# Performance work log

Measured on AMD Instinct MI355X. Metric: run time of the kernel, lower is better.

Reference implementation:

```python
import jax, jax.numpy as jnp
import numpy as np

B, T, H, NUM_LAYERS = 256, 1024, 128, 2


def _lstm_layer(x, W_ih, W_hh, b_ih, b_hh):
    """Single LSTM layer, PyTorch gate order (i, f, g, o).
    x: [B, T, in], W_ih: [4H, in], W_hh: [4H, H], biases: [4H]. Returns [B, T, H].
    """
    Bv = x.shape[0]
    Hv = W_hh.shape[1]
    # Precompute input-to-gate projections for all timesteps (big GEMM outside scan)
    xg = jnp.einsum('bti,gi->btg', x, W_ih) + b_ih + b_hh  # [B, T, 4H]

    def step(carry, xg_t):
        h, c = carry
        g = xg_t + h @ W_hh.T  # [B, 4H]
        i, f, gg, o = jnp.split(g, 4, axis=-1)
        i = jax.nn.sigmoid(i)
        f = jax.nn.sigmoid(f)
        gg = jnp.tanh(gg)
        o = jax.nn.sigmoid(o)
        c = f * c + i * gg
        h = o * jnp.tanh(c)
        return (h, c), h

    h0 = jnp.zeros((Bv, Hv), x.dtype)
    c0 = jnp.zeros((Bv, Hv), x.dtype)
    _, hs = jax.lax.scan(step, (h0, c0), jnp.swapaxes(xg, 0, 1))  # hs: [T, B, H]
    return jnp.swapaxes(hs, 0, 1)


def setup_inputs() -> dict:
    key = jax.random.key(0)
    ks = jax.random.split(key, 11)
    s = 1.0 / np.sqrt(H)  # PyTorch LSTM init scale
    inp = {
        'x': jax.random.normal(ks[0], (B, T, 1), dtype=jnp.float32),
        'W_ih0': jax.random.uniform(ks[1], (4 * H, 1), minval=-s, maxval=s, dtype=jnp.float32),
        'W_hh0': jax.random.uniform(ks[2], (4 * H, H), minval=-s, maxval=s, dtype=jnp.float32),
        'b_ih0': jax.random.uniform(ks[3], (4 * H,), minval=-s, maxval=s, dtype=jnp.float32),
        'b_hh0': jax.random.uniform(ks[4], (4 * H,), minval=-s, maxval=s, dtype=jnp.float32),
        'W_ih1': jax.random.uniform(ks[5], (4 * H, H), minval=-s, maxval=s, dtype=jnp.float32),
        'W_hh1': jax.random.uniform(ks[6], (4 * H, H), minval=-s, maxval=s, dtype=jnp.float32),
        'b_ih1': jax.random.uniform(ks[7], (4 * H,), minval=-s, maxval=s, dtype=jnp.float32),
        'b_hh1': jax.random.uniform(ks[8], (4 * H,), minval=-s, maxval=s, dtype=jnp.float32),
        'fc_w': jax.random.uniform(ks[9], (1, H), minval=-s, maxval=s, dtype=jnp.float32),
        'fc_b': jax.random.uniform(ks[10], (1,), minval=-s, maxval=s, dtype=jnp.float32),
    }
    return inp


def reference(x, W_ih0, W_hh0, b_ih0, b_hh0, W_ih1, W_hh1, b_ih1, b_hh1, fc_w, fc_b):
    h = _lstm_layer(x, W_ih0, W_hh0, b_ih0, b_hh0)   # [B, T, H]
    h = _lstm_layer(h, W_ih1, W_hh1, b_ih1, b_hh1)   # [B, T, H]
    out = jnp.einsum('bth,oh->bto', h, fc_w) + fc_b  # [B, T, 1]
    return out
```

## Files before the change

kernel.cpp:

```cpp
#include <hip/hip_runtime.h>

#define TT 1024
#define HH 128

typedef unsigned int u32;
typedef unsigned short u16;
typedef _Float16 f16;
typedef f16 f16x2 __attribute__((ext_vector_type(2)));
typedef f16 f16x8 __attribute__((ext_vector_type(8)));
typedef float f32x4 __attribute__((ext_vector_type(4)));
typedef u32 u32x4 __attribute__((ext_vector_type(4)));

#define MFMA16(A, B, C) __builtin_amdgcn_mfma_f32_16x16x32_f16((A), (B), (C), 0, 0, 0)
#define K2L2E 2.8853900817779268f

__device__ __forceinline__ float ex2(float x) {
#if __has_builtin(__builtin_amdgcn_exp2f)
    return __builtin_amdgcn_exp2f(x);
#else
    extern "C" __device__ float __ocml_exp2_f32(float);
    return __ocml_exp2_f32(x);
#endif
}
__device__ __forceinline__ float rcp_(float x) { return __builtin_amdgcn_rcpf(x); }

__device__ __forceinline__ float fdot2_(u32 w, u32 h, float acc) {
#if __has_builtin(__builtin_amdgcn_fdot2)
    return __builtin_amdgcn_fdot2(__builtin_bit_cast(f16x2, w),
                                  __builtin_bit_cast(f16x2, h), acc, false);
#else
    const f16x2 a = __builtin_bit_cast(f16x2, w);
    const f16x2 b = __builtin_bit_cast(f16x2, h);
    return fmaf((float)a.y, (float)b.y, fmaf((float)a.x, (float)b.x, acc));
#endif
}

__device__ __forceinline__ float dpp_mov(float v, const int ctrl) {
    int t;
    switch (ctrl) {
      case 0x00: t = __builtin_amdgcn_update_dpp(0, __float_as_int(v), 0x00, 0xF, 0xF, true); break;
      case 0x55: t = __builtin_amdgcn_update_dpp(0, __float_as_int(v), 0x55, 0xF, 0xF, true); break;
      case 0xAA: t = __builtin_amdgcn_update_dpp(0, __float_as_int(v), 0xAA, 0xF, 0xF, true); break;
      default:   t = __builtin_amdgcn_update_dpp(0, __float_as_int(v), 0xFF, 0xF, 0xF, true); break;
    }
    return __int_as_float(t);
}
__device__ __forceinline__ float dpp_add(float v, const int ctrl) {
    int t;
    switch (ctrl) {
      case 0xB1:  t = __builtin_amdgcn_update_dpp(0, __float_as_int(v), 0xB1,  0xF, 0xF, true); break;
      case 0x4E:  t = __builtin_amdgcn_update_dpp(0, __float_as_int(v), 0x4E,  0xF, 0xF, true); break;
      default:    t = __builtin_amdgcn_update_dpp(0, __float_as_int(v), 0x141, 0xF, 0xF, true); break;
    }
    return v + __int_as_float(t);
}
__device__ __forceinline__ float red8(float v) {
    v = dpp_add(v, 0xB1); v = dpp_add(v, 0x4E); v = dpp_add(v, 0x141);
    return v;
}

__global__ void prep(const float* __restrict__ Whh0, const float* __restrict__ Whh1,
                     const float* __restrict__ Wih1, const float* __restrict__ Wih0,
                     const float* __restrict__ bih0, const float* __restrict__ bhh0,
                     const float* __restrict__ bih1, const float* __restrict__ bhh1,
                     f16* __restrict__ Wpk0, f16* __restrict__ Wpk1,
                     f16* __restrict__ W1h,  f16* __restrict__ W1l,
                     float* __restrict__ bx0, float* __restrict__ wx0,
                     float* __restrict__ b1p)
{
    const int p = blockIdx.x;
    const int k = threadIdx.x;
    const int c = p & 3, u = p >> 2;
    const int g = c * 128 + u;
    const float sc = (c == 2) ? K2L2E : -1.4426950408889634f;

    Wpk0[p * HH + k] = (f16)(Whh0[(size_t)g * HH + k] * sc);
    Wpk1[p * HH + k] = (f16)(Whh1[(size_t)g * HH + k] * sc);
    const float wf = Wih1[(size_t)g * HH + k] * sc;
    const f16 wh = (f16)wf;
    W1h[p * HH + k] = wh;
    W1l[p * HH + k] = (f16)(wf - (float)wh);
    if (k == 0) {
        bx0[p] = (bih0[g] + bhh0[g]) * sc;
        wx0[p] = Wih0[g] * sc;
        b1p[p] = (bih1[g] + bhh1[g]) * sc;
    }
}

__global__ __launch_bounds__(512, 2) void lstm0(
    const float* __restrict__ x, const f16* __restrict__ Wpk0,
    const float* __restrict__ bx0, const float* __restrict__ wx0,
    f16* __restrict__ h0g)
{
    const int b = blockIdx.x;
    const int tid = threadIdx.x;
    const int u = tid >> 2;
    const bool lead = (tid & 3) == 0;
    const bool is_g = (tid & 3) == 2;
    const float Ag = is_g ? -2.f : 1.f;
    const float Cg = is_g ?  1.f : 0.f;

    __shared__ __align__(16) float xS[TT];
    __shared__ __align__(16) u32 hS[2][64];
    __shared__ __align__(16) u16 hO[32][HH];

    xS[tid] = x[(size_t)b * TT + tid];
    xS[tid + 512] = x[(size_t)b * TT + tid + 512];
    if (tid < 128) hS[0][tid & 63] = 0u;

    u32x4 Wv[16];
    {
        const u32* wp = (const u32*)(Wpk0 + (size_t)tid * HH);
#pragma unroll
        for (int r = 0; r < 16; ++r) Wv[r] = *(const u32x4*)(wp + r * 4);
    }
    const float biasx = bx0[tid];
    const float wxv = wx0[tid];
    float c1 = 0.f;
    __syncthreads();

    f16* og = h0g + (size_t)b * TT * HH;

#pragma unroll 1
    for (int t0 = 0; t0 < TT; t0 += 32) {
#pragma unroll 1
        for (int i = 0; i < 32; ++i) {
            const int t = t0 + i;
            const u32* hcur = hS[t & 1];
            float a0 = 0.f, a1 = 0.f;
#pragma unroll
            for (int r = 0; r < 16; ++r) {
                const u32x4 hq = *(const u32x4*)(hcur + r * 4);
                a0 = fdot2_(Wv[r].x, hq.x, a0);
                a1 = fdot2_(Wv[r].y, hq.y, a1);
                a0 = fdot2_(Wv[r].z, hq.z, a0);
                a1 = fdot2_(Wv[r].w, hq.w, a1);
            }
            const float a = a0 + a1 + fmaf(xS[t], wxv, biasx);
            const float act = fmaf(Ag, rcp_(1.f + ex2(a)), Cg);
            const float gi = dpp_mov(act, 0x00);
            const float gf = dpp_mov(act, 0x55);
            const float gg = dpp_mov(act, 0xAA);
            const float go = dpp_mov(act, 0xFF);
            c1 = fmaf(gf, c1, gi * gg);
            const float h = go * fmaf(-2.f, rcp_(1.f + ex2(K2L2E * c1)), 1.f);
            if (lead) {
                const u16 hb = __builtin_bit_cast(u16, (f16)h);
                ((u16*)hS[(t + 1) & 1])[u] = hb;
                hO[i][u] = hb;
            }
            __syncthreads();
        }
        *(u32x4*)((u16*)og + (size_t)t0 * HH + tid * 8) = *(const u32x4*)(&hO[0][0] + tid * 8);
        __syncthreads();
    }
}

__global__ __launch_bounds__(512, 2) void lstm1(
    const f16* __restrict__ h0g, const f16* __restrict__ Wpk1,
    const f16* __restrict__ W1h, const f16* __restrict__ W1l,
    const float* __restrict__ b1p, const float* __restrict__ fcw,
    const float* __restrict__ fcb, float* __restrict__ out)
{
    const int b = blockIdx.x;
    const int tid = threadIdx.x;
    const int u = tid >> 2;
    const int wv = tid >> 6;
    const int lane = tid & 63;
    const int lr = lane & 15, lq = lane >> 4;
    const bool lead = (tid & 3) == 0;
    const bool is_g = (tid & 3) == 2;
    const float Ag = is_g ? -2.f : 1.f;
    const float Cg = is_g ?  1.f : 0.f;

    __shared__ __align__(16) float xgS[32 * 512];
    __shared__ __align__(16) u32 hS[2][64];
    __shared__ __align__(16) float fcP[2][8];

    if (tid < 128) hS[0][tid & 63] = 0u;
    const float fcwv = fcw[u];
    const float fcbv = fcb[0];
    const int bp_addr = ((lane ^ 32) << 2);
    float c1 = 0.f;
    __syncthreads();

    const f16* hb0 = h0g + (size_t)b * TT * HH;
    float* ob = out + (size_t)b * TT;

#pragma unroll 1
    for (int t0 = 0; t0 < TT; t0 += 32) {
        {
            f16x8 B0[4], B1[4];
#pragma unroll
            for (int ks = 0; ks < 4; ++ks) {
                B0[ks] = *(const f16x8*)(hb0 + (size_t)(t0 + lr) * HH + ks * 32 + lq * 8);
                B1[ks] = *(const f16x8*)(hb0 + (size_t)(t0 + 16 + lr) * HH + ks * 32 + lq * 8);
            }
#pragma unroll
            for (int gtl = 0; gtl < 4; ++gtl) {
                const int g16 = (wv * 4 + gtl) * 16;
                const float4 bi = *(const float4*)&b1p[g16 + lq * 4];
                f32x4 a0 = {bi.x, bi.y, bi.z, bi.w};
                f32x4 a1 = a0;
#pragma unroll
                for (int ks = 0; ks < 4; ++ks) {
                    const f16x8 Ah = *(const f16x8*)(W1h + (size_t)(g16 + lr) * HH + ks * 32 + lq * 8);
                    const f16x8 Al = *(const f16x8*)(W1l + (size_t)(g16 + lr) * HH + ks * 32 + lq * 8);
                    a0 = MFMA16(Ah, B0[ks], a0);
                    a0 = MFMA16(Al, B0[ks], a0);
                    a1 = MFMA16(Ah, B1[ks], a1);
                    a1 = MFMA16(Al, B1[ks], a1);
                }
                const int gb = g16 + lq * 4;
                *(f32x4*)&xgS[lr * 512 + (gb ^ ((lr & 7) << 2))] = a0;
                *(f32x4*)&xgS[(16 + lr) * 512 + (gb ^ (((16 + lr) & 7) << 2))] = a1;
            }
        }
        __syncthreads();

        u32x4 Wv[16];
        {
            const u32* wp = (const u32*)(Wpk1 + (size_t)tid * HH);
            asm volatile("" : "+v"(wp));
#pragma unroll
            for (int r = 0; r < 16; ++r) Wv[r] = *(const u32x4*)(wp + r * 4);
        }

#pragma unroll 1
        for (int i = 0; i < 32; ++i) {
            const int t = t0 + i;
            if (wv == 7 && t > 0) {
                float v = (lane < 8) ? fcP[(t & 1) ^ 1][lane] : 0.f;
                v = red8(v);
                if (lane == 0) ob[t - 1] = v + fcbv;
            }
            const u32* hcur = hS[t & 1];
            float a0 = 0.f, a1 = 0.f;
#pragma unroll
            for (int r = 0; r < 16; ++r) {
                const u32x4 hq = *(const u32x4*)(hcur + r * 4);
                a0 = fdot2_(Wv[r].x, hq.x, a0);
                a1 = fdot2_(Wv[r].y, hq.y, a1);
                a0 = fdot2_(Wv[r].z, hq.z, a0);
                a1 = fdot2_(Wv[r].w, hq.w, a1);
            }
            const float a = a0 + a1 + xgS[i * 512 + (tid ^ ((i & 7) << 2))];
            const float act = fmaf(Ag, rcp_(1.f + ex2(a)), Cg);
            const float gi = dpp_mov(act, 0x00);
            const float gf = dpp_mov(act, 0x55);
            const float gg = dpp_mov(act, 0xAA);
            const float go = dpp_mov(act, 0xFF);
            c1 = fmaf(gf, c1, gi * gg);
            const float h = go * fmaf(-2.f, rcp_(1.f + ex2(K2L2E * c1)), 1.f);
            if (lead) ((u16*)hS[(t + 1) & 1])[u] = __builtin_bit_cast(u16, (f16)h);
            float pf = lead ? h * fcwv : 0.f;
            pf = red8(pf);
            pf += __int_as_float(__builtin_amdgcn_ds_swizzle(__float_as_int(pf), 0x201F));
            pf += __int_as_float(__builtin_amdgcn_ds_swizzle(__float_as_int(pf), 0x401F));
            pf += __int_as_float(__builtin_amdgcn_ds_bpermute(bp_addr, __float_as_int(pf)));
            if (lane == 0) fcP[t & 1][wv] = pf;
            __syncthreads();
        }
    }
    if (wv == 7) {
        float v = (lane < 8) ? fcP[(TT - 1) & 1][lane] : 0.f;
        v = red8(v);
        if (lane == 0) ob[TT - 1] = v + fcbv;
    }
}

extern "C" void kernel_launch(void* const* d_in, const int* in_sizes, int n_in,
                              void* d_out, int out_size, void* d_ws, size_t ws_size,
                              hipStream_t stream)
{
    const float* x    = (const float*)d_in[0];
    const float* Wih0 = (const float*)d_in[1];
    const float* Whh0 = (const float*)d_in[2];
    const float* bih0 = (const float*)d_in[3];
    const float* bhh0 = (const float*)d_in[4];
    const float* Wih1 = (const float*)d_in[5];
    const float* Whh1 = (const float*)d_in[6];
    const float* bih1 = (const float*)d_in[7];
    const float* bhh1 = (const float*)d_in[8];
    const float* fcw  = (const float*)d_in[9];
    const float* fcb  = (const float*)d_in[10];
    float* out = (float*)d_out;

    f16* h0g  = (f16*)d_ws;
    f16* Wpk0 = h0g + (size_t)256 * TT * HH;
    f16* Wpk1 = Wpk0 + 512 * HH;
    f16* W1h  = Wpk1 + 512 * HH;
    f16* W1l  = W1h + 512 * HH;
    float* bx0 = (float*)(W1l + 512 * HH);
    float* wx0 = bx0 + 512;
    float* b1p = wx0 + 512;

    prep <<<512, 128, 0, stream>>>(Whh0, Whh1, Wih1, Wih0, bih0, bhh0, bih1, bhh1,
                                   Wpk0, Wpk1, W1h, W1l, bx0, wx0, b1p);
    lstm0<<<256, 512, 0, stream>>>(x, Wpk0, bx0, wx0, h0g);
    lstm1<<<256, 512, 0, stream>>>(h0g, Wpk1, W1h, W1l, b1p, fcw, fcb, out);
}
```

Before: 1.447 ms.

## Fuse both LSTM layers into one wavefront-pipelined kernel

Merges the two per-layer recurrent kernels into one kernel that runs layer 0 on chunk c while layer 1 runs on chunk c-1. Both layers advance inside the same per-timestep barrier. Layer-0 hidden states stay in shared memory (swizzled) and feed the MFMA input projection directly, removing the global h0 round trip and one long serial kernel. The cost is twice the register weights per thread, occupancy bound dropping to 1 block per CU, and more work per barrier step. The fc output reduction is also moved to read h1 from shared memory one step later.

Result: slower. 1.533 ms (+6.0%).

```diff
diff --git a/kernel.cpp b/kernel.cpp
--- a/kernel.cpp
+++ b/kernel.cpp
@@ -87,114 +87,136 @@
     }
 }
 
-__global__ __launch_bounds__(512, 2) void lstm0(
-    const float* __restrict__ x, const f16* __restrict__ Wpk0,
-    const float* __restrict__ bx0, const float* __restrict__ wx0,
-    f16* __restrict__ h0g)
-{
-    const int b = blockIdx.x;
-    const int tid = threadIdx.x;
-    const int u = tid >> 2;
-    const bool lead = (tid & 3) == 0;
-    const bool is_g = (tid & 3) == 2;
-    const float Ag = is_g ? -2.f : 1.f;
-    const float Cg = is_g ?  1.f : 0.f;
-
-    __shared__ __align__(16) float xS[TT];
-    __shared__ __align__(16) u32 hS[2][64];
-    __shared__ __align__(16) u16 hO[32][HH];
-
-    xS[tid] = x[(size_t)b * TT + tid];
-    xS[tid + 512] = x[(size_t)b * TT + tid + 512];
-    if (tid < 128) hS[0][tid & 63] = 0u;
-
-    u32x4 Wv[16];
-    {
-        const u32* wp = (const u32*)(Wpk0 + (size_t)tid * HH);
-#pragma unroll
-        for (int r = 0; r < 16; ++r) Wv[r] = *(const u32x4*)(wp + r * 4);
-    }
-    const float biasx = bx0[tid];
-    const float wxv = wx0[tid];
-    float c1 = 0.f;
-    __syncthreads();
-
-    f16* og = h0g + (size_t)b * TT * HH;
-
-#pragma unroll 1
-    for (int t0 = 0; t0 < TT; t0 += 32) {
-#pragma unroll 1
-        for (int i = 0; i < 32; ++i) {
-            const int t = t0 + i;
-            const u32* hcur = hS[t & 1];
-            float a0 = 0.f, a1 = 0.f;
-#pragma unroll
-            for (int r = 0; r < 16; ++r) {
-                const u32x4 hq = *(const u32x4*)(hcur + r * 4);
-                a0 = fdot2_(Wv[r].x, hq.x, a0);
-                a1 = fdot2_(Wv[r].y, hq.y, a1);
-                a0 = fdot2_(Wv[r].z, hq.z, a0);
-                a1 = fdot2_(Wv[r].w, hq.w, a1);
-            }
-            const float a = a0 + a1 + fmaf(xS[t], wxv, biasx);
-            const float act = fmaf(Ag, rcp_(1.f + ex2(a)), Cg);
-            const float gi = dpp_mov(act, 0x00);
-            const float gf = dpp_mov(act, 0x55);
-            const float gg = dpp_mov(act, 0xAA);
-            const float go = dpp_mov(act, 0xFF);
-            c1 = fmaf(gf, c1, gi * gg);
-            const float h = go * fmaf(-2.f, rcp_(1.f + ex2(K2L2E * c1)), 1.f);
-            if (lead) {
-                const u16 hb = __builtin_bit_cast(u16, (f16)h);
-                ((u16*)hS[(t + 1) & 1])[u] = hb;
-                hO[i][u] = hb;
-            }
-            __syncthreads();
-        }
-        *(u32x4*)((u16*)og + (size_t)t0 * HH + tid * 8) = *(const u32x4*)(&hO[0][0] + tid * 8);
-        __syncthreads();
-    }
-}
-
-__global__ __launch_bounds__(512, 2) void lstm1(
-    const f16* __restrict__ h0g, const f16* __restrict__ Wpk1,
-    const f16* __restrict__ W1h, const f16* __restrict__ W1l,
+__global__ __launch_bounds__(512, 1) void lstm_fused(
+    const float* __restrict__ x,
+    const f16* __restrict__ Wpk0, const float* __restrict__ bx0,
+    const float* __restrict__ wx0, const f16* __restrict__ Wpk1,
+    const f16* __restrict__ W1h,  const f16* __restrict__ W1l,
     const float* __restrict__ b1p, const float* __restrict__ fcw,
     const float* __restrict__ fcb, float* __restrict__ out)
 {
     const int b = blockIdx.x;
     const int tid = threadIdx.x;
     const int u = tid >> 2;
-    const int wv = tid >> 6;
-    const int lane = tid & 63;
+    const int wv = tid >> 6, lane = tid & 63;
     const int lr = lane & 15, lq = lane >> 4;
     const bool lead = (tid & 3) == 0;
     const bool is_g = (tid & 3) == 2;
     const float Ag = is_g ? -2.f : 1.f;
     const float Cg = is_g ?  1.f : 0.f;
 
+    __shared__ __align__(16) float xS[TT];
     __shared__ __align__(16) float xgS[32 * 512];
-    __shared__ __align__(16) u32 hS[2][64];
-    __shared__ __align__(16) float fcP[2][8];
-
-    if (tid < 128) hS[0][tid & 63] = 0u;
-    const float fcwv = fcw[u];
-    const float fcbv = fcb[0];
+    __shared__ __align__(16) u16 h0c[32][HH];
+    __shared__ __align__(16) u32 hS0[2][64];
+    __shared__ __align__(16) u32 hS1[2][64];
+
+    xS[tid]       = x[(size_t)b * TT + tid];
+    xS[tid + 512] = x[(size_t)b * TT + tid + 512];
+    if (tid < 64) { hS0[0][tid] = 0u; hS0[1][tid] = 0u; hS1[0][tid] = 0u; hS1[1][tid] = 0u; }
+
+    u32x4 W0[16], W1r[16];
+    {
+        const u32* wp0 = (const u32*)(Wpk0 + (size_t)tid * HH);
+        const u32* wp1 = (const u32*)(Wpk1 + (size_t)tid * HH);
+#pragma unroll
+        for (int r = 0; r < 16; ++r) {
+            W0[r]  = *(const u32x4*)(wp0 + r * 4);
+            W1r[r] = *(const u32x4*)(wp1 + r * 4);
+        }
+    }
+    const float biasx = bx0[tid];
+    const float wxv   = wx0[tid];
+    const float2 fc2  = *(const float2*)&fcw[2 * lane];
+    const float fcbv  = fcb[0];
     const int bp_addr = ((lane ^ 32) << 2);
-    float c1 = 0.f;
+    float c0 = 0.f, c1 = 0.f;
+    float* ob = out + (size_t)b * TT;
     __syncthreads();
 
-    const f16* hb0 = h0g + (size_t)b * TT * HH;
-    float* ob = out + (size_t)b * TT;
-
 #pragma unroll 1
-    for (int t0 = 0; t0 < TT; t0 += 32) {
-        {
+    for (int cc = 0; cc < 33; ++cc) {
+        const bool l0act = cc < 32;
+        const bool l1act = cc > 0;
+        const int t0 = cc * 32;
+
+#pragma unroll 1
+        for (int i = 0; i < 32; ++i) {
+            const int cur = i & 1, nxt = cur ^ 1;
+            const int t1 = t0 - 32 + i;
+
+            if (l1act && wv == 7 && t1 > 0) {
+                const f16x2 hp = __builtin_bit_cast(f16x2, hS1[cur][lane]);
+                float pf = fmaf((float)hp.y, fc2.y, (float)hp.x * fc2.x);
+                pf = red8(pf);
+                pf += __int_as_float(__builtin_amdgcn_ds_swizzle(__float_as_int(pf), 0x201F));
+                pf += __int_as_float(__builtin_amdgcn_ds_swizzle(__float_as_int(pf), 0x401F));
+                pf += __int_as_float(__builtin_amdgcn_ds_bpermute(bp_addr, __float_as_int(pf)));
+                if (lane == 0) ob[t1 - 1] = pf + fcbv;
+            }
+
+            float h0v = 0.f;
+            if (l0act) {
+                const u32* hcur = hS0[cur];
+                float a0 = 0.f, a1 = 0.f, a2 = 0.f, a3 = 0.f;
+#pragma unroll
+                for (int r = 0; r < 16; ++r) {
+                    const u32x4 hq = *(const u32x4*)(hcur + r * 4);
+                    a0 = fdot2_(W0[r].x, hq.x, a0);
+                    a1 = fdot2_(W0[r].y, hq.y, a1);
+                    a2 = fdot2_(W0[r].z, hq.z, a2);
+                    a3 = fdot2_(W0[r].w, hq.w, a3);
+                }
+                const float a = (a0 + a1) + (a2 + a3) + fmaf(xS[t0 + i], wxv, biasx);
+                const float act = fmaf(Ag, rcp_(1.f + ex2(a)), Cg);
+                const float gi = dpp_mov(act, 0x00);
+                const float gf = dpp_mov(act, 0x55);
+                const float gg = dpp_mov(act, 0xAA);
+                const float go = dpp_mov(act, 0xFF);
+                c0 = fmaf(gf, c0, gi * gg);
+                h0v = go * fmaf(-2.f, rcp_(1.f + ex2(K2L2E * c0)), 1.f);
+            }
+
+            float h1v = 0.f;
+            if (l1act) {
+                const float xgv = xgS[i * 512 + (tid ^ ((i & 7) << 2))];
+                const u32* hcur = hS1[cur];
+                float a0 = 0.f, a1 = 0.f, a2 = 0.f, a3 = 0.f;
+#pragma unroll
+                for (int r = 0; r < 16; ++r) {
+                    const u32x4 hq = *(const u32x4*)(hcur + r * 4);
+                    a0 = fdot2_(W1r[r].x, hq.x, a0);
+                    a1 = fdot2_(W1r[r].y, hq.y, a1);
+                    a2 = fdot2_(W1r[r].z, hq.z, a2);
+                    a3 = fdot2_(W1r[r].w, hq.w, a3);
+                }
+                const float a = (a0 + a1) + (a2 + a3) + xgv;
+                const float act = fmaf(Ag, rcp_(1.f + ex2(a)), Cg);
+                const float gi = dpp_mov(act, 0x00);
+                const float gf = dpp_mov(act, 0x55);
+                const float gg = dpp_mov(act, 0xAA);
+                const float go = dpp_mov(act, 0xFF);
+                c1 = fmaf(gf, c1, gi * gg);
+                h1v = go * fmaf(-2.f, rcp_(1.f + ex2(K2L2E * c1)), 1.f);
+            }
+
+            if (l0act && lead) {
+                const u16 hb = __builtin_bit_cast(u16, (f16)h0v);
+                ((u16*)hS0[nxt])[u] = hb;
+                h0c[i][u ^ ((i & 7) << 3)] = hb;
+            }
+            if (l1act && lead)
+                ((u16*)hS1[nxt])[u] = __builtin_bit_cast(u16, (f16)h1v);
+            __syncthreads();
+        }
+
+        if (l0act) {
             f16x8 B0[4], B1[4];
 #pragma unroll
             for (int ks = 0; ks < 4; ++ks) {
-                B0[ks] = *(const f16x8*)(hb0 + (size_t)(t0 + lr) * HH + ks * 32 + lq * 8);
-                B1[ks] = *(const f16x8*)(hb0 + (size_t)(t0 + 16 + lr) * HH + ks * 32 + lq * 8);
+                const int kb = (ks * 32 + lq * 8) ^ ((lr & 7) << 3);
+                B0[ks] = *(const f16x8*)&h0c[lr][kb];
+                B1[ks] = *(const f16x8*)&h0c[16 + lr][kb];
             }
 #pragma unroll
             for (int gtl = 0; gtl < 4; ++gtl) {
@@ -213,59 +235,20 @@
                 }
                 const int gb = g16 + lq * 4;
                 *(f32x4*)&xgS[lr * 512 + (gb ^ ((lr & 7) << 2))] = a0;
-                *(f32x4*)&xgS[(16 + lr) * 512 + (gb ^ (((16 + lr) & 7) << 2))] = a1;
+                *(f32x4*)&xgS[(16 + lr) * 512 + (gb ^ ((lr & 7) << 2))] = a1;
             }
         }
         __syncthreads();
-
-        u32x4 Wv[16];
-        {
-            const u32* wp = (const u32*)(Wpk1 + (size_t)tid * HH);
-            asm volatile("" : "+v"(wp));
-#pragma unroll
-            for (int r = 0; r < 16; ++r) Wv[r] = *(const u32x4*)(wp + r * 4);
-        }
-
-#pragma unroll 1
-        for (int i = 0; i < 32; ++i) {
-            const int t = t0 + i;
-            if (wv == 7 && t > 0) {
-                float v = (lane < 8) ? fcP[(t & 1) ^ 1][lane] : 0.f;
-                v = red8(v);
-                if (lane == 0) ob[t - 1] = v + fcbv;
-            }
-            const u32* hcur = hS[t & 1];
-            float a0 = 0.f, a1 = 0.f;
-#pragma unroll
-            for (int r = 0; r < 16; ++r) {
-                const u32x4 hq = *(const u32x4*)(hcur + r * 4);
-                a0 = fdot2_(Wv[r].x, hq.x, a0);
-                a1 = fdot2_(Wv[r].y, hq.y, a1);
-                a0 = fdot2_(Wv[r].z, hq.z, a0);
-                a1 = fdot2_(Wv[r].w, hq.w, a1);
-            }
-            const float a = a0 + a1 + xgS[i * 512 + (tid ^ ((i & 7) << 2))];
-            const float act = fmaf(Ag, rcp_(1.f + ex2(a)), Cg);
-            const float gi = dpp_mov(act, 0x00);
-            const float gf = dpp_mov(act, 0x55);
-            const float gg = dpp_mov(act, 0xAA);
-            const float go = dpp_mov(act, 0xFF);
-            c1 = fmaf(gf, c1, gi * gg);
-            const float h = go * fmaf(-2.f, rcp_(1.f + ex2(K2L2E * c1)), 1.f);
-            if (lead) ((u16*)hS[(t + 1) & 1])[u] = __builtin_bit_cast(u16, (f16)h);
-            float pf = lead ? h * fcwv : 0.f;
-            pf = red8(pf);
-            pf += __int_as_float(__builtin_amdgcn_ds_swizzle(__float_as_int(pf), 0x201F));
-            pf += __int_as_float(__builtin_amdgcn_ds_swizzle(__float_as_int(pf), 0x401F));
-            pf += __int_as_float(__builtin_amdgcn_ds_bpermute(bp_addr, __float_as_int(pf)));
-            if (lane == 0) fcP[t & 1][wv] = pf;
-            __syncthreads();
-        }
-    }
+    }
+
     if (wv == 7) {
-        float v = (lane < 8) ? fcP[(TT - 1) & 1][lane] : 0.f;
-        v = red8(v);
-        if (lane == 0) ob[TT - 1] = v + fcbv;
+        const f16x2 hp = __builtin_bit_cast(f16x2, hS1[0][lane]);
+        float pf = fmaf((float)hp.y, fc2.y, (float)hp.x * fc2.x);
+        pf = red8(pf);
+        pf += __int_as_float(__builtin_amdgcn_ds_swizzle(__float_as_int(pf), 0x201F));
+        pf += __int_as_float(__builtin_amdgcn_ds_swizzle(__float_as_int(pf), 0x401F));
+        pf += __int_as_float(__builtin_amdgcn_ds_bpermute(bp_addr, __float_as_int(pf)));
+        if (lane == 0) ob[TT - 1] = pf + fcbv;
     }
 }
 
@@ -286,8 +269,7 @@
     const float* fcb  = (const float*)d_in[10];
     float* out = (float*)d_out;
 
-    f16* h0g  = (f16*)d_ws;
-    f16* Wpk0 = h0g + (size_t)256 * TT * HH;
+    f16* Wpk0 = (f16*)d_ws;
     f16* Wpk1 = Wpk0 + 512 * HH;
     f16* W1h  = Wpk1 + 512 * HH;
     f16* W1l  = W1h + 512 * HH;
@@ -295,8 +277,8 @@
     float* wx0 = bx0 + 512;
     float* b1p = wx0 + 512;
 
-    prep <<<512, 128, 0, stream>>>(Whh0, Whh1, Wih1, Wih0, bih0, bhh0, bih1, bhh1,
-                                   Wpk0, Wpk1, W1h, W1l, bx0, wx0, b1p);
-    lstm0<<<256, 512, 0, stream>>>(x, Wpk0, bx0, wx0, h0g);
-    lstm1<<<256, 512, 0, stream>>>(h0g, Wpk1, W1h, W1l, b1p, fcw, fcb, out);
-}
+    prep<<<512, 128, 0, stream>>>(Whh0, Whh1, Wih1, Wih0, bih0, bhh0, bih1, bhh1,
+                                  Wpk0, Wpk1, W1h, W1l, bx0, wx0, b1p);
+    lstm_fused<<<256, 512, 0, stream>>>(x, Wpk0, bx0, wx0, Wpk1, W1h, W1l, b1p,
+                                        fcw, fcb, out);
+}
```

## Split recurrent dot products across quad lanes with DPP transpose-reduce, batch FC output

Applied to the files above, without the earlier changes.

Each thread in a 4-lane group now computes partial dot products over one quarter of K for all four gates of its hidden unit, then combines them with a DPP butterfly transpose-reduce. Before, each thread ran a full 128-long K loop for a single gate. The hidden-state LDS layout is swizzled so the four lanes read different banks, and layer 0's step loop is flattened. In layer 1, the per-step FC reduction drops the ds_bpermute and serial wave-7 output and instead writes partials per step, which 32 threads sum once per 32-step chunk. This aims to shorten the serial per-step dependency chain at the cost of extra DPP shuffles and selects.

Measured after the change: 1.269 ms. 12.3% less time.

```diff
diff --git a/kernel.cpp b/kernel.cpp
--- a/kernel.cpp
+++ b/kernel.cpp
@@ -41,7 +41,9 @@
       case 0x00: t = __builtin_amdgcn_update_dpp(0, __float_as_int(v), 0x00, 0xF, 0xF, true); break;
       case 0x55: t = __builtin_amdgcn_update_dpp(0, __float_as_int(v), 0x55, 0xF, 0xF, true); break;
       case 0xAA: t = __builtin_amdgcn_update_dpp(0, __float_as_int(v), 0xAA, 0xF, 0xF, true); break;
-      default:   t = __builtin_amdgcn_update_dpp(0, __float_as_int(v), 0xFF, 0xF, 0xF, true); break;
+      case 0xFF: t = __builtin_amdgcn_update_dpp(0, __float_as_int(v), 0xFF, 0xF, 0xF, true); break;
+      case 0xB1: t = __builtin_amdgcn_update_dpp(0, __float_as_int(v), 0xB1, 0xF, 0xF, true); break;
+      default:   t = __builtin_amdgcn_update_dpp(0, __float_as_int(v), 0x4E, 0xF, 0xF, true); break;
     }
     return __int_as_float(t);
 }
@@ -50,13 +52,30 @@
     switch (ctrl) {
       case 0xB1:  t = __builtin_amdgcn_update_dpp(0, __float_as_int(v), 0xB1,  0xF, 0xF, true); break;
       case 0x4E:  t = __builtin_amdgcn_update_dpp(0, __float_as_int(v), 0x4E,  0xF, 0xF, true); break;
-      default:    t = __builtin_amdgcn_update_dpp(0, __float_as_int(v), 0x141, 0xF, 0xF, true); break;
+      case 0x141: t = __builtin_amdgcn_update_dpp(0, __float_as_int(v), 0x141, 0xF, 0xF, true); break;
+      default:    t = __builtin_amdgcn_update_dpp(0, __float_as_int(v), 0x140, 0xF, 0xF, true); break;
     }
     return v + __int_as_float(t);
 }
-__device__ __forceinline__ float red8(float v) {
-    v = dpp_add(v, 0xB1); v = dpp_add(v, 0x4E); v = dpp_add(v, 0x141);
-    return v;
+
+__device__ __forceinline__ int hswz(int iu) {
+    return (iu & 0x30) + (((((iu >> 2) & 3) + (iu >> 4)) & 3) << 2) + (iu & 3);
+}
+
+__device__ __forceinline__ float xpose4(float a0, float a1, float a2, float a3, int q) {
+    const bool qb0 = (q & 1) != 0;
+    float s0, s1;
+    {
+        const float send = qb0 ? a0 : a1;
+        s0 = (qb0 ? a1 : a0) + dpp_mov(send, 0xB1);
+    }
+    {
+        const float send = qb0 ? a2 : a3;
+        s1 = (qb0 ? a3 : a2) + dpp_mov(send, 0xB1);
+    }
+    const bool qb1 = (q & 2) != 0;
+    const float send = qb1 ? s0 : s1;
+    return (qb1 ? s1 : s0) + dpp_mov(send, 0x4E);
 }
 
 __global__ void prep(const float* __restrict__ Whh0, const float* __restrict__ Whh1,
@@ -94,9 +113,8 @@
 {
     const int b = blockIdx.x;
     const int tid = threadIdx.x;
-    const int u = tid >> 2;
-    const bool lead = (tid & 3) == 0;
-    const bool is_g = (tid & 3) == 2;
+    const int u = tid >> 2, q = tid & 3;
+    const bool is_g = (q == 2);
     const float Ag = is_g ? -2.f : 1.f;
     const float Cg = is_g ?  1.f : 0.f;
 
@@ -104,55 +122,60 @@
     __shared__ __align__(16) u32 hS[2][64];
     __shared__ __align__(16) u16 hO[32][HH];
 
-    xS[tid] = x[(size_t)b * TT + tid];
+    xS[tid]       = x[(size_t)b * TT + tid];
     xS[tid + 512] = x[(size_t)b * TT + tid + 512];
-    if (tid < 128) hS[0][tid & 63] = 0u;
-
-    u32x4 Wv[16];
-    {
-        const u32* wp = (const u32*)(Wpk0 + (size_t)tid * HH);
-#pragma unroll
-        for (int r = 0; r < 16; ++r) Wv[r] = *(const u32x4*)(wp + r * 4);
+    if (tid < 128) ((u32*)hS)[tid] = 0u;
+
+    u32x4 Wq[4][4];
+#pragma unroll
+    for (int c = 0; c < 4; ++c) {
+        const u32* wp = (const u32*)Wpk0 + (size_t)((tid & ~3) + c) * 64 + q * 16;
+#pragma unroll
+        for (int rb = 0; rb < 4; ++rb) Wq[c][rb] = *(const u32x4*)(wp + rb * 4);
     }
     const float biasx = bx0[tid];
-    const float wxv = wx0[tid];
+    const float wxv   = wx0[tid];
     float c1 = 0.f;
     __syncthreads();
 
     f16* og = h0g + (size_t)b * TT * HH;
 
 #pragma unroll 1
-    for (int t0 = 0; t0 < TT; t0 += 32) {
-#pragma unroll 1
-        for (int i = 0; i < 32; ++i) {
-            const int t = t0 + i;
-            const u32* hcur = hS[t & 1];
-            float a0 = 0.f, a1 = 0.f;
-#pragma unroll
-            for (int r = 0; r < 16; ++r) {
-                const u32x4 hq = *(const u32x4*)(hcur + r * 4);
-                a0 = fdot2_(Wv[r].x, hq.x, a0);
-                a1 = fdot2_(Wv[r].y, hq.y, a1);
-                a0 = fdot2_(Wv[r].z, hq.z, a0);
-                a1 = fdot2_(Wv[r].w, hq.w, a1);
-            }
-            const float a = a0 + a1 + fmaf(xS[t], wxv, biasx);
-            const float act = fmaf(Ag, rcp_(1.f + ex2(a)), Cg);
-            const float gi = dpp_mov(act, 0x00);
-            const float gf = dpp_mov(act, 0x55);
-            const float gg = dpp_mov(act, 0xAA);
-            const float go = dpp_mov(act, 0xFF);
-            c1 = fmaf(gf, c1, gi * gg);
-            const float h = go * fmaf(-2.f, rcp_(1.f + ex2(K2L2E * c1)), 1.f);
-            if (lead) {
-                const u16 hb = __builtin_bit_cast(u16, (f16)h);
-                ((u16*)hS[(t + 1) & 1])[u] = hb;
-                hO[i][u] = hb;
-            }
+    for (int t = 0; t < TT; ++t) {
+        const u32* hcur = hS[t & 1];
+        float a0 = 0.f, a1 = 0.f, a2 = 0.f, a3 = 0.f;
+#pragma unroll
+        for (int rb = 0; rb < 4; ++rb) {
+            const u32x4 hq = *(const u32x4*)(hcur + (q << 4) + (((rb + q) & 3) << 2));
+            a0 = fdot2_(Wq[0][rb].x, hq.x, a0); a0 = fdot2_(Wq[0][rb].y, hq.y, a0);
+            a0 = fdot2_(Wq[0][rb].z, hq.z, a0); a0 = fdot2_(Wq[0][rb].w, hq.w, a0);
+            a1 = fdot2_(Wq[1][rb].x, hq.x, a1); a1 = fdot2_(Wq[1][rb].y, hq.y, a1);
+            a1 = fdot2_(Wq[1][rb].z, hq.z, a1); a1 = fdot2_(Wq[1][rb].w, hq.w, a1);
+            a2 = fdot2_(Wq[2][rb].x, hq.x, a2); a2 = fdot2_(Wq[2][rb].y, hq.y, a2);
+            a2 = fdot2_(Wq[2][rb].z, hq.z, a2); a2 = fdot2_(Wq[2][rb].w, hq.w, a2);
+            a3 = fdot2_(Wq[3][rb].x, hq.x, a3); a3 = fdot2_(Wq[3][rb].y, hq.y, a3);
+            a3 = fdot2_(Wq[3][rb].z, hq.z, a3); a3 = fdot2_(Wq[3][rb].w, hq.w, a3);
+        }
+        const float V = xpose4(a0, a1, a2, a3, q);
+        const float a = V + fmaf(xS[t], wxv, biasx);
+        const float act = fmaf(Ag, rcp_(1.f + ex2(a)), Cg);
+        const float gi = dpp_mov(act, 0x00);
+        const float gf = dpp_mov(act, 0x55);
+        const float gg = dpp_mov(act, 0xAA);
+        const float go = dpp_mov(act, 0xFF);
+        c1 = fmaf(gf, c1, gi * gg);
+        const float h = go * fmaf(-2.f, rcp_(1.f + ex2(K2L2E * c1)), 1.f);
+        if (q == 0) {
+            const u16 hb = __builtin_bit_cast(u16, (f16)h);
+            ((u16*)hS[(t + 1) & 1])[2 * hswz(u >> 1) + (u & 1)] = hb;
+            hO[t & 31][u] = hb;
+        }
+        __syncthreads();
+        if ((t & 31) == 31) {
+            *(u32x4*)((u16*)og + (size_t)(t - 31) * HH + tid * 8) =
+                *(const u32x4*)(&hO[0][0] + tid * 8);
             __syncthreads();
         }
-        *(u32x4*)((u16*)og + (size_t)t0 * HH + tid * 8) = *(const u32x4*)(&hO[0][0] + tid * 8);
-        __syncthreads();
     }
 }
 
@@ -164,23 +187,20 @@
 {
     const int b = blockIdx.x;
     const int tid = threadIdx.x;
-    const int u = tid >> 2;
-    const int wv = tid >> 6;
-    const int lane = tid & 63;
+    const int u = tid >> 2, q = tid & 3;
+    const int wv = tid >> 6, lane = tid & 63;
     const int lr = lane & 15, lq = lane >> 4;
-    const bool lead = (tid & 3) == 0;
-    const bool is_g = (tid & 3) == 2;
+    const bool is_g = (q == 2);
     const float Ag = is_g ? -2.f : 1.f;
     const float Cg = is_g ?  1.f : 0.f;
 
     __shared__ __align__(16) float xgS[32 * 512];
-    __shared__ __align__(16) u32 hS[2][64];
-    __shared__ __align__(16) float fcP[2][8];
-
-    if (tid < 128) hS[0][tid & 63] = 0u;
-    const float fcwv = fcw[u];
+    __shared__ __align__(16) u32 hS1[2][64];
+    __shared__ __align__(16) float fcP[32][16];
+
+    if (tid < 128) ((u32*)hS1)[tid] = 0u;
+    const float fcu025 = fcw[u] * 0.25f;
     const float fcbv = fcb[0];
-    const int bp_addr = ((lane ^ 32) << 2);
     float c1 = 0.f;
     __syncthreads();
 
@@ -213,38 +233,42 @@
                 }
                 const int gb = g16 + lq * 4;
                 *(f32x4*)&xgS[lr * 512 + (gb ^ ((lr & 7) << 2))] = a0;
-                *(f32x4*)&xgS[(16 + lr) * 512 + (gb ^ (((16 + lr) & 7) << 2))] = a1;
+                *(f32x4*)&xgS[(16 + lr) * 512 + (gb ^ ((lr & 7) << 2))] = a1;
             }
         }
         __syncthreads();
 
-        u32x4 Wv[16];
+        u32x4 Wq[4][4];
         {
-            const u32* wp = (const u32*)(Wpk1 + (size_t)tid * HH);
-            asm volatile("" : "+v"(wp));
-#pragma unroll
-            for (int r = 0; r < 16; ++r) Wv[r] = *(const u32x4*)(wp + r * 4);
+            const u32* wb = (const u32*)Wpk1;
+            asm volatile("" : "+v"(wb));
+#pragma unroll
+            for (int c = 0; c < 4; ++c) {
+                const u32* wp = wb + (size_t)((tid & ~3) + c) * 64 + q * 16;
+#pragma unroll
+                for (int rb = 0; rb < 4; ++rb) Wq[c][rb] = *(const u32x4*)(wp + rb * 4);
+            }
         }
 
 #pragma unroll 1
         for (int i = 0; i < 32; ++i) {
             const int t = t0 + i;
-            if (wv == 7 && t > 0) {
-                float v = (lane < 8) ? fcP[(t & 1) ^ 1][lane] : 0.f;
-                v = red8(v);
-                if (lane == 0) ob[t - 1] = v + fcbv;
-            }
-            const u32* hcur = hS[t & 1];
-            float a0 = 0.f, a1 = 0.f;
-#pragma unroll
-            for (int r = 0; r < 16; ++r) {
-                const u32x4 hq = *(const u32x4*)(hcur + r * 4);
-                a0 = fdot2_(Wv[r].x, hq.x, a0);
-                a1 = fdot2_(Wv[r].y, hq.y, a1);
-                a0 = fdot2_(Wv[r].z, hq.z, a0);
-                a1 = fdot2_(Wv[r].w, hq.w, a1);
-            }
-            const float a = a0 + a1 + xgS[i * 512 + (tid ^ ((i & 7) << 2))];
+            const u32* hcur = hS1[t & 1];
+            float a0 = 0.f, a1 = 0.f, a2 = 0.f, a3 = 0.f;
+#pragma unroll
+            for (int rb = 0; rb < 4; ++rb) {
+                const u32x4 hq = *(const u32x4*)(hcur + (q << 4) + (((rb + q) & 3) << 2));
+                a0 = fdot2_(Wq[0][rb].x, hq.x, a0); a0 = fdot2_(Wq[0][rb].y, hq.y, a0);
+                a0 = fdot2_(Wq[0][rb].z, hq.z, a0); a0 = fdot2_(Wq[0][rb].w, hq.w, a0);
+                a1 = fdot2_(Wq[1][rb].x, hq.x, a1); a1 = fdot2_(Wq[1][rb].y, hq.y, a1);
+                a1 = fdot2_(Wq[1][rb].z, hq.z, a1); a1 = fdot2_(Wq[1][rb].w, hq.w, a1);
+                a2 = fdot2_(Wq[2][rb].x, hq.x, a2); a2 = fdot2_(Wq[2][rb].y, hq.y, a2);
+                a2 = fdot2_(Wq[2][rb].z, hq.z, a2); a2 = fdot2_(Wq[2][rb].w, hq.w, a2);
+                a3 = fdot2_(Wq[3][rb].x, hq.x, a3); a3 = fdot2_(Wq[3][rb].y, hq.y, a3);
+                a3 = fdot2_(Wq[3][rb].z, hq.z, a3); a3 = fdot2_(Wq[3][rb].w, hq.w, a3);
+            }
+            const float V = xpose4(a0, a1, a2, a3, q);
+            const float a = V + xgS[i * 512 + (tid ^ ((i & 7) << 2))];
             const float act = fmaf(Ag, rcp_(1.f + ex2(a)), Cg);
             const float gi = dpp_mov(act, 0x00);
             const float gf = dpp_mov(act, 0x55);
@@ -252,20 +276,29 @@
             const float go = dpp_mov(act, 0xFF);
             c1 = fmaf(gf, c1, gi * gg);
             const float h = go * fmaf(-2.f, rcp_(1.f + ex2(K2L2E * c1)), 1.f);
-            if (lead) ((u16*)hS[(t + 1) & 1])[u] = __builtin_bit_cast(u16, (f16)h);
-            float pf = lead ? h * fcwv : 0.f;
-            pf = red8(pf);
-            pf += __int_as_float(__builtin_amdgcn_ds_swizzle(__float_as_int(pf), 0x201F));
+            if (q == 0)
+                ((u16*)hS1[(t + 1) & 1])[2 * hswz(u >> 1) + (u & 1)] =
+                    __builtin_bit_cast(u16, (f16)h);
+
+            float pf = h * fcu025;
+            pf = dpp_add(pf, 0xB1);
+            pf = dpp_add(pf, 0x4E);
+            pf = dpp_add(pf, 0x141);
+            pf = dpp_add(pf, 0x140);
             pf += __int_as_float(__builtin_amdgcn_ds_swizzle(__float_as_int(pf), 0x401F));
-            pf += __int_as_float(__builtin_amdgcn_ds_bpermute(bp_addr, __float_as_int(pf)));
-            if (lane == 0) fcP[t & 1][wv] = pf;
+            if ((lane & 31) == 0) fcP[i][wv * 2 + (lane >> 5)] = pf;
             __syncthreads();
         }
-    }
-    if (wv == 7) {
-        float v = (lane < 8) ? fcP[(TT - 1) & 1][lane] : 0.f;
-        v = red8(v);
-        if (lane == 0) ob[TT - 1] = v + fcbv;
+
+        if (tid < 32) {
+            float s = 0.f;
+#pragma unroll
+            for (int r = 0; r < 4; ++r) {
+                const float4 v = *(const float4*)&fcP[tid][r * 4];
+                s += (v.x + v.y) + (v.z + v.w);
+            }
+            ob[t0 + tid] = s + fcbv;
+        }
     }
 }
 
```
